# Kernel optimization log

Measured on AMD Instinct MI355X. Metric: run time of the kernel, lower is better.

## Reference

```python
import jax, jax.numpy as jnp
import numpy as np

N, E = 100000, 1000000
IN_DIM, OUT_DIM, HEADS = 64, 64, 4
C = OUT_DIM // HEADS  # per-head channels = 16
NEG_SLOPE = 0.2
SOFTMAX_EPS = 1e-16  # PyG softmax denominator epsilon
LN_EPS = 1e-5


def setup_inputs() -> dict:
    key = jax.random.key(0)
    ks = jax.random.split(key, 8)
    node_input = jax.random.normal(ks[0], (N, IN_DIM), dtype=jnp.float32)
    edge_index = jax.random.randint(ks[1], (2, E), 0, N, dtype=jnp.int64)
    # GATConv params (glorot-ish scale)
    W = jax.random.normal(ks[2], (IN_DIM, HEADS * C), dtype=jnp.float32) / np.sqrt(IN_DIM)
    att_src = jax.random.normal(ks[3], (HEADS, C), dtype=jnp.float32) / np.sqrt(C)
    att_dst = jax.random.normal(ks[4], (HEADS, C), dtype=jnp.float32) / np.sqrt(C)
    bias = jnp.zeros((HEADS * C,), dtype=jnp.float32)
    # LayerNorm params
    gamma = jnp.ones((OUT_DIM,), dtype=jnp.float32)
    beta = jnp.zeros((OUT_DIM,), dtype=jnp.float32)
    return {"node_input": node_input, "edge_index": edge_index, "W": W,
            "att_src": att_src, "att_dst": att_dst, "bias": bias,
            "gamma": gamma, "beta": beta}


def _gat_forward(x, edge_index, W, att_src, att_dst, bias, gamma, beta):
    src, dst = edge_index[0], edge_index[1]  # message flows src -> dst
    h = (x @ W).reshape(N, HEADS, C)                       # [N, H, C]
    a_src = jnp.einsum('nhc,hc->nh', h, att_src)           # [N, H]
    a_dst = jnp.einsum('nhc,hc->nh', h, att_dst)           # [N, H]
    # per-edge attention logits + leaky relu
    e = a_src[src] + a_dst[dst]                            # [E, H]
    e = jnp.where(e >= 0, e, NEG_SLOPE * e)
    # segment softmax over incoming edges of each target node
    m = jax.ops.segment_max(e, dst, num_segments=N)        # [N, H]
    m = jnp.where(jnp.isfinite(m), m, 0.0)                 # empty segments -> 0
    ex = jnp.exp(e - m[dst])                               # [E, H]
    denom = jax.ops.segment_sum(ex, dst, num_segments=N)   # [N, H]
    alpha = ex / (denom[dst] + SOFTMAX_EPS)                # [E, H]
    # weighted scatter-sum of source features
    msg = alpha[:, :, None] * h[src]                       # [E, H, C]
    out = jax.ops.segment_sum(msg, dst, num_segments=N)    # [N, H, C]
    out = out.reshape(N, HEADS * C) + bias                 # concat heads + bias
    # LayerNorm
    mu = out.mean(axis=-1, keepdims=True)
    var = out.var(axis=-1, keepdims=True)
    out = (out - mu) * jax.lax.rsqrt(var + LN_EPS) * gamma + beta
    # query gate is dead code (graph is a dict -> hasattr fails); dropout is eval identity
    return out


def reference(node_input, edge_index, W, att_src, att_dst, bias, gamma, beta):
    return _gat_forward(node_input, edge_index, W, att_src, att_dst, bias, gamma, beta)
```

## Files before the change

kernel.cpp:

```cpp
#include <hip/hip_runtime.h>
#include <hip/hip_bf16.h>
#include <math.h>

#define N_NODES 100000
#define E_EDGES 1000000
#define HEADS 4
#define DIM 64
#define NEG_SLOPE 0.2f
#define SM_EPS 1e-16f
#define LN_EPS 1e-5f
#define P1_BLOCKS 256
#define NT16 6250
#define GEMM_BLOCKS 1563
#define FEAT_BLOCKS (P1_BLOCKS + GEMM_BLOCKS)
#define CHUNK 3907
#define EPT 16
#define BUCKET_W 512
#define NBUCK 196
#define CAP 48

typedef __attribute__((ext_vector_type(8))) short short8v;
typedef __attribute__((ext_vector_type(4))) float f32x4;

static __device__ __forceinline__ unsigned short bfh(float f) {
    __hip_bfloat16 b = __float2bfloat16(f);
    return *reinterpret_cast<unsigned short*>(&b);
}
static __device__ __forceinline__ float bfh2f(unsigned short u) {
    return __uint_as_float((unsigned)u << 16);
}

__global__ __launch_bounds__(256) void k_wprep(
        const float* __restrict__ W, uint4* __restrict__ Wf) {
    int t = threadIdx.x;
    for (int e = t; e < 1024; e += 256) {
        int l = e & 63, f = e >> 6;
        int s = f & 1, kh = (f >> 1) & 1, n = f >> 2;
        int c = n * 16 + (l & 15);
        int k0 = kh * 32 + (l >> 4) * 8;
        unsigned short hw[8];
#pragma unroll
        for (int j = 0; j < 8; ++j) {
            float wv = W[(k0 + j) * 64 + c];
            unsigned short hi = bfh(wv);
            hw[j] = s ? bfh(wv - bfh2f(hi)) : hi;
        }
        uint4 pk;
        pk.x = hw[0] | ((unsigned)hw[1] << 16);
        pk.y = hw[2] | ((unsigned)hw[3] << 16);
        pk.z = hw[4] | ((unsigned)hw[5] << 16);
        pk.w = hw[6] | ((unsigned)hw[7] << 16);
        Wf[e] = pk;
    }
}

__global__ __launch_bounds__(256) void k_feat(
        const float* __restrict__ x, const float* __restrict__ Wf_,
        const float* __restrict__ att_src, const float* __restrict__ att_dst,
        const int* __restrict__ ei, __hip_bfloat16* __restrict__ hb,
        float* __restrict__ asrc, float* __restrict__ adst,
        int2* __restrict__ chunkbuf, int* __restrict__ pre) {
    __shared__ __align__(16) int smem_i[8326];
    int t = threadIdx.x;

    if (blockIdx.x < P1_BLOCKS) {
        int2* out2 = (int2*)smem_i;
        int*  cnt  = smem_i + 2 * CHUNK;
        int*  scan = cnt + 256;
        int base_e = blockIdx.x * CHUNK;
        int es[EPT], ed[EPT];
#pragma unroll
        for (int k = 0; k < EPT; ++k) {
            int i = k * 256 + t;
            int e = base_e + i;
            bool v = (i < CHUNK) && (e < E_EDGES);
            es[k] = v ? ei[e] : 0;
            ed[k] = v ? ei[E_EDGES + e] : -1;
        }
        cnt[t] = 0;
        __syncthreads();
#pragma unroll
        for (int k = 0; k < EPT; ++k)
            if (ed[k] >= 0) atomicAdd(&cnt[ed[k] >> 9], 1);
        __syncthreads();
        scan[t] = (t < NBUCK) ? cnt[t] : 0;
        __syncthreads();
#pragma unroll
        for (int off = 1; off < 256; off <<= 1) {
            int v = (t >= off) ? scan[t - off] : 0;
            __syncthreads();
            scan[t] += v;
            __syncthreads();
        }
        int excl = (t == 0) ? 0 : scan[t - 1];
        if (t < NBUCK) pre[blockIdx.x * (NBUCK + 1) + t] = excl;
        if (t == 0)    pre[blockIdx.x * (NBUCK + 1) + NBUCK] = scan[NBUCK - 1];
        if (t < NBUCK) cnt[t] = excl;
        __syncthreads();
#pragma unroll
        for (int k = 0; k < EPT; ++k)
            if (ed[k] >= 0) {
                int pos = atomicAdd(&cnt[ed[k] >> 9], 1);
                out2[pos] = make_int2(es[k], ed[k]);
            }
        __syncthreads();
        int ec = E_EDGES - base_e; ec = (ec > CHUNK) ? CHUNK : ec;
        for (int i = t; i < ec; i += 256)
            chunkbuf[base_e + i] = out2[i];
        return;
    }

    int w = t >> 6, lane = t & 63;
    int tile = (blockIdx.x - P1_BLOCKS) * 4 + w;
    if (tile >= NT16) return;
    int base = tile * 16;
    int m = lane & 15, kg = lane >> 4;

    const float* xr = x + (size_t)(base + m) * 64 + kg * 8;
    short8v ah[2], al[2];
#pragma unroll
    for (int kh = 0; kh < 2; ++kh) {
        float4 q0 = *(const float4*)(xr + kh * 32);
        float4 q1 = *(const float4*)(xr + kh * 32 + 4);
        float qq[8] = {q0.x, q0.y, q0.z, q0.w, q1.x, q1.y, q1.z, q1.w};
#pragma unroll
        for (int j = 0; j < 8; ++j) {
            unsigned short h = bfh(qq[j]);
            ah[kh][j] = (short)h;
            al[kh][j] = (short)bfh(qq[j] - bfh2f(h));
        }
    }

    const short8v* Wfv = (const short8v*)Wf_;
    float vs_keep = 0.f, vd_keep = 0.f;
#pragma unroll
    for (int n = 0; n < 4; ++n) {
        short8v bh0 = Wfv[((n * 2 + 0) * 2 + 0) * 64 + lane];
        short8v bl0 = Wfv[((n * 2 + 0) * 2 + 1) * 64 + lane];
        short8v bh1 = Wfv[((n * 2 + 1) * 2 + 0) * 64 + lane];
        short8v bl1 = Wfv[((n * 2 + 1) * 2 + 1) * 64 + lane];
        f32x4 a4 = {0.f, 0.f, 0.f, 0.f};
        a4 = __builtin_amdgcn_mfma_f32_16x16x32_bf16(ah[0], bh0, a4, 0, 0, 0);
        a4 = __builtin_amdgcn_mfma_f32_16x16x32_bf16(al[0], bh0, a4, 0, 0, 0);
        a4 = __builtin_amdgcn_mfma_f32_16x16x32_bf16(ah[0], bl0, a4, 0, 0, 0);
        a4 = __builtin_amdgcn_mfma_f32_16x16x32_bf16(ah[1], bh1, a4, 0, 0, 0);
        a4 = __builtin_amdgcn_mfma_f32_16x16x32_bf16(al[1], bh1, a4, 0, 0, 0);
        a4 = __builtin_amdgcn_mfma_f32_16x16x32_bf16(ah[1], bl1, a4, 0, 0, 0);
        float asv = att_src[n * 16 + m];
        float adv = att_dst[n * 16 + m];
#pragma unroll
        for (int ri = 0; ri < 4; ++ri) {
            int orow = base + kg * 4 + ri;
            hb[(size_t)orow * 64 + n * 16 + m] = __float2bfloat16(a4[ri]);
            float p = a4[ri] * asv, pd = a4[ri] * adv;
#pragma unroll
            for (int off = 1; off < 16; off <<= 1) {
                p  += __shfl_xor(p,  off, 64);
                pd += __shfl_xor(pd, off, 64);
            }
            if (m == ri * 4 + n) { vs_keep = p; vd_keep = pd; }
        }
    }
    asrc[tile * 64 + kg * 16 + m] = vs_keep;
    adst[tile * 64 + kg * 16 + m] = vd_keep;
}

__global__ __launch_bounds__(256) void k_bin2(
        const int2* __restrict__ chunkbuf, const int* __restrict__ pre,
        int* __restrict__ cursor, int* __restrict__ srclist) {
    __shared__ int cnt2[BUCKET_W];
    __shared__ int segstart[P1_BLOCKS];
    __shared__ int segpre[P1_BLOCKS + 1];
    __shared__ int scan[P1_BLOCKS];
    int t = threadIdx.x;
    int b = blockIdx.x;
    int base = b * BUCKET_W;
    for (int i = t; i < BUCKET_W; i += 256) cnt2[i] = 0;
    int p0 = pre[t * (NBUCK + 1) + b];
    int p1 = pre[t * (NBUCK + 1) + b + 1];
    segstart[t] = t * CHUNK + p0;
    scan[t] = p1 - p0;
    __syncthreads();
#pragma unroll
    for (int off = 1; off < 256; off <<= 1) {
        int v = (t >= off) ? scan[t - off] : 0;
        __syncthreads();
        scan[t] += v;
        __syncthreads();
    }
    segpre[t + 1] = scan[t];
    if (t == 0) segpre[0] = 0;
    __syncthreads();
    int total = segpre[P1_BLOCKS];
    for (int i = t; i < total; i += 256) {
        int lo = 0, hi = P1_BLOCKS;
#pragma unroll
        for (int it = 0; it < 8; ++it) {
            int mid = (lo + hi) >> 1;
            if (segpre[mid] <= i) lo = mid; else hi = mid;
        }
        int2 e = chunkbuf[segstart[lo] + (i - segpre[lo])];
        int pos = atomicAdd(&cnt2[e.y - base], 1);
        if (pos < CAP) srclist[e.y * CAP + pos] = e.x;
    }
    __syncthreads();
    for (int i = t; i < BUCKET_W; i += 256) {
        int node = base + i;
        if (node < N_NODES) cursor[node] = cnt2[i];
    }
}

__global__ __launch_bounds__(256) void k_aggr(
        const int* __restrict__ cursor, const int* __restrict__ srclist,
        const float* __restrict__ asrc, const float* __restrict__ adst,
        const __hip_bfloat16* __restrict__ hb,
        const float* __restrict__ bias, const float* __restrict__ gamma,
        const float* __restrict__ beta, float* __restrict__ out) {
    int t = threadIdx.x;
    int node = blockIdx.x * 4 + (t >> 6);
    int lane = t & 63;
    int q = lane >> 4, j = lane & 15;
    int hd = j >> 2;
    int dcnt = cursor[node];
    dcnt = (dcnt > CAP) ? CAP : dcnt;
    const int* sl = srclist + node * CAP;
    const ushort4* hp = (const ushort4*)hb;
    float ad = adst[node * HEADS + hd];
    float acc0 = 0.f, acc1 = 0.f, acc2 = 0.f, acc3 = 0.f, l = 0.f;

    for (int i0 = 0; i0 < dcnt; i0 += 16) {
        int idx[4];
        float as[4];
        ushort4 hv[4];
#pragma unroll
        for (int k = 0; k < 4; ++k) {
            int ek = i0 + 4 * k + q;
            idx[k] = (ek < dcnt) ? sl[ek] : 0;
        }
#pragma unroll
        for (int k = 0; k < 4; ++k) as[k] = asrc[idx[k] * HEADS + hd];
#pragma unroll
        for (int k = 0; k < 4; ++k) hv[k] = hp[idx[k] * 16 + j];
#pragma unroll
        for (int k = 0; k < 4; ++k) {
            int ek = i0 + 4 * k + q;
            float e = as[k] + ad;
            e = (e >= 0.f) ? e : NEG_SLOPE * e;
            float p = (ek < dcnt) ? __expf(e) : 0.f;
            l += p;
            acc0 += p * __uint_as_float((unsigned)hv[k].x << 16);
            acc1 += p * __uint_as_float((unsigned)hv[k].y << 16);
            acc2 += p * __uint_as_float((unsigned)hv[k].z << 16);
            acc3 += p * __uint_as_float((unsigned)hv[k].w << 16);
        }
    }
    acc0 += __shfl_xor(acc0, 16, 64); acc0 += __shfl_xor(acc0, 32, 64);
    acc1 += __shfl_xor(acc1, 16, 64); acc1 += __shfl_xor(acc1, 32, 64);
    acc2 += __shfl_xor(acc2, 16, 64); acc2 += __shfl_xor(acc2, 32, 64);
    acc3 += __shfl_xor(acc3, 16, 64); acc3 += __shfl_xor(acc3, 32, 64);
    l    += __shfl_xor(l,    16, 64); l    += __shfl_xor(l,    32, 64);

    float inv = 1.f / (l + SM_EPS);
    float4 b4 = ((const float4*)bias)[j];
    float v0 = acc0 * inv + b4.x;
    float v1 = acc1 * inv + b4.y;
    float v2 = acc2 * inv + b4.z;
    float v3 = acc3 * inv + b4.w;
    float s1 = (v0 + v1) + (v2 + v3);
    float s2 = (v0 * v0 + v1 * v1) + (v2 * v2 + v3 * v3);
#pragma unroll
    for (int off = 1; off < 16; off <<= 1) {
        s1 += __shfl_xor(s1, off, 64);
        s2 += __shfl_xor(s2, off, 64);
    }
    float mu = s1 * (1.f / 64.f);
    float var = s2 * (1.f / 64.f) - mu * mu;
    float r = rsqrtf(var + LN_EPS);
    if (q == 0) {
        float4 g4 = ((const float4*)gamma)[j];
        float4 be4 = ((const float4*)beta)[j];
        float4 o;
        o.x = (v0 - mu) * r * g4.x + be4.x;
        o.y = (v1 - mu) * r * g4.y + be4.y;
        o.z = (v2 - mu) * r * g4.z + be4.z;
        o.w = (v3 - mu) * r * g4.w + be4.w;
        ((float4*)(out + (size_t)node * DIM))[j] = o;
    }
}

extern "C" void kernel_launch(void* const* d_in, const int* in_sizes, int n_in,
                              void* d_out, int out_size, void* d_ws, size_t ws_size,
                              hipStream_t stream) {
    const float* x       = (const float*)d_in[0];
    const int*   ei      = (const int*)d_in[1];
    const float* W       = (const float*)d_in[2];
    const float* att_src = (const float*)d_in[3];
    const float* att_dst = (const float*)d_in[4];
    const float* bias    = (const float*)d_in[5];
    const float* gamma   = (const float*)d_in[6];
    const float* beta    = (const float*)d_in[7];
    float* out = (float*)d_out;

    int2* chunkbuf = (int2*)d_ws;
    int*  pre      = (int*)(chunkbuf + (size_t)P1_BLOCKS * CHUNK);
    int*  cursor   = pre + (size_t)P1_BLOCKS * (NBUCK + 1);
    int*  srclist  = cursor + N_NODES;
    float* asrc    = (float*)(srclist + (size_t)N_NODES * CAP);
    float* adst    = asrc + (size_t)N_NODES * HEADS;
    __hip_bfloat16* hb = (__hip_bfloat16*)(adst + (size_t)N_NODES * HEADS);
    uint4* Wf      = (uint4*)(hb + (size_t)N_NODES * DIM);

    k_wprep<<<1, 256, 0, stream>>>(W, Wf);
    k_feat<<<FEAT_BLOCKS, 256, 0, stream>>>(x, (const float*)Wf, att_src,
                                            att_dst, ei, hb, asrc, adst,
                                            chunkbuf, pre);
    k_bin2<<<NBUCK, 256, 0, stream>>>(chunkbuf, pre, cursor, srclist);
    k_aggr<<<N_NODES / 4, 256, 0, stream>>>(cursor, srclist, asrc, adst, hb,
                                            bias, gamma, beta, out);
}
```

Baseline: 167.2 us.

## Build compact CSR source lists and pack two nodes per wavefront in aggregation

The binning kernel now runs two passes over each bucket's edges. The first pass counts in-degree per node, then an in-block prefix scan plus a global bucket offset gives exact CSR offsets, packed with the degree into one cursor word. This replaces the fixed 48-slot padded per-node list, which shrinks the source-list footprint and removes the silent cap. The aggregation kernel now gives each wavefront two nodes of 32 lanes each, iterating to the larger of the two degrees, so low-degree nodes waste fewer lanes. In exchange, binning reads the chunk buffer twice, and the packed word limits the degree to 63.

```diff
diff --git a/kernel.cpp b/kernel.cpp
--- a/kernel.cpp
+++ b/kernel.cpp
@@ -17,7 +17,6 @@
 #define EPT 16
 #define BUCKET_W 512
 #define NBUCK 196
-#define CAP 48
 
 typedef __attribute__((ext_vector_type(8))) short short8v;
 typedef __attribute__((ext_vector_type(4))) float f32x4;
@@ -167,18 +166,29 @@
 
 __global__ __launch_bounds__(256) void k_bin2(
         const int2* __restrict__ chunkbuf, const int* __restrict__ pre,
-        int* __restrict__ cursor, int* __restrict__ srclist) {
+        int* __restrict__ cursorP, int* __restrict__ srclist) {
     __shared__ int cnt2[BUCKET_W];
     __shared__ int segstart[P1_BLOCKS];
     __shared__ int segpre[P1_BLOCKS + 1];
     __shared__ int scan[P1_BLOCKS];
     int t = threadIdx.x;
     int b = blockIdx.x;
-    int base = b * BUCKET_W;
+    int nbase = b * BUCKET_W;
     for (int i = t; i < BUCKET_W; i += 256) cnt2[i] = 0;
     int p0 = pre[t * (NBUCK + 1) + b];
     int p1 = pre[t * (NBUCK + 1) + b + 1];
     segstart[t] = t * CHUNK + p0;
+    scan[t] = p0;
+    __syncthreads();
+#pragma unroll
+    for (int off = 128; off >= 1; off >>= 1) {
+        int v = (t < off) ? scan[t + off] : 0;
+        __syncthreads();
+        if (t < off) scan[t] += v;
+        __syncthreads();
+    }
+    int gbase = scan[0];
+    __syncthreads();
     scan[t] = p1 - p0;
     __syncthreads();
 #pragma unroll
@@ -200,41 +210,65 @@
             if (segpre[mid] <= i) lo = mid; else hi = mid;
         }
         int2 e = chunkbuf[segstart[lo] + (i - segpre[lo])];
-        int pos = atomicAdd(&cnt2[e.y - base], 1);
-        if (pos < CAP) srclist[e.y * CAP + pos] = e.x;
-    }
-    __syncthreads();
-    for (int i = t; i < BUCKET_W; i += 256) {
-        int node = base + i;
-        if (node < N_NODES) cursor[node] = cnt2[i];
+        atomicAdd(&cnt2[e.y - nbase], 1);
+    }
+    __syncthreads();
+    int c0 = cnt2[2 * t], c1 = cnt2[2 * t + 1];
+    scan[t] = c0 + c1;
+    __syncthreads();
+#pragma unroll
+    for (int off = 1; off < 256; off <<= 1) {
+        int v = (t >= off) ? scan[t - off] : 0;
+        __syncthreads();
+        scan[t] += v;
+        __syncthreads();
+    }
+    int pexcl = (t == 0) ? 0 : scan[t - 1];
+    cnt2[2 * t]     = pexcl;
+    cnt2[2 * t + 1] = pexcl + c0;
+    int n0 = nbase + 2 * t;
+    if (n0 < N_NODES)     cursorP[n0]     = ((gbase + pexcl) << 6) | c0;
+    if (n0 + 1 < N_NODES) cursorP[n0 + 1] = ((gbase + pexcl + c0) << 6) | c1;
+    __syncthreads();
+    for (int i = t; i < total; i += 256) {
+        int lo = 0, hi = P1_BLOCKS;
+#pragma unroll
+        for (int it = 0; it < 8; ++it) {
+            int mid = (lo + hi) >> 1;
+            if (segpre[mid] <= i) lo = mid; else hi = mid;
+        }
+        int2 e = chunkbuf[segstart[lo] + (i - segpre[lo])];
+        int pos = atomicAdd(&cnt2[e.y - nbase], 1);
+        srclist[gbase + pos] = e.x;
     }
 }
 
 __global__ __launch_bounds__(256) void k_aggr(
-        const int* __restrict__ cursor, const int* __restrict__ srclist,
+        const int* __restrict__ cursorP, const int* __restrict__ srclist,
         const float* __restrict__ asrc, const float* __restrict__ adst,
         const __hip_bfloat16* __restrict__ hb,
         const float* __restrict__ bias, const float* __restrict__ gamma,
         const float* __restrict__ beta, float* __restrict__ out) {
     int t = threadIdx.x;
-    int node = blockIdx.x * 4 + (t >> 6);
     int lane = t & 63;
-    int q = lane >> 4, j = lane & 15;
+    int s = lane >> 5, qq = (lane >> 4) & 1, j = lane & 15;
     int hd = j >> 2;
-    int dcnt = cursor[node];
-    dcnt = (dcnt > CAP) ? CAP : dcnt;
-    const int* sl = srclist + node * CAP;
+    int node = blockIdx.x * 8 + (t >> 6) * 2 + s;
+    int cw = cursorP[node];
+    int dcnt = cw & 63;
+    const int* sl = srclist + ((unsigned)cw >> 6);
+    int dmax = max(dcnt, __shfl_xor(dcnt, 32, 64));
     const ushort4* hp = (const ushort4*)hb;
     float ad = adst[node * HEADS + hd];
     float acc0 = 0.f, acc1 = 0.f, acc2 = 0.f, acc3 = 0.f, l = 0.f;
 
-    for (int i0 = 0; i0 < dcnt; i0 += 16) {
+    for (int i0 = 0; i0 < dmax; i0 += 8) {
         int idx[4];
         float as[4];
         ushort4 hv[4];
 #pragma unroll
         for (int k = 0; k < 4; ++k) {
-            int ek = i0 + 4 * k + q;
+            int ek = i0 + 2 * k + qq;
             idx[k] = (ek < dcnt) ? sl[ek] : 0;
         }
 #pragma unroll
@@ -243,7 +277,7 @@
         for (int k = 0; k < 4; ++k) hv[k] = hp[idx[k] * 16 + j];
 #pragma unroll
         for (int k = 0; k < 4; ++k) {
-            int ek = i0 + 4 * k + q;
+            int ek = i0 + 2 * k + qq;
             float e = as[k] + ad;
             e = (e >= 0.f) ? e : NEG_SLOPE * e;
             float p = (ek < dcnt) ? __expf(e) : 0.f;
@@ -254,11 +288,11 @@
             acc3 += p * __uint_as_float((unsigned)hv[k].w << 16);
         }
     }
-    acc0 += __shfl_xor(acc0, 16, 64); acc0 += __shfl_xor(acc0, 32, 64);
-    acc1 += __shfl_xor(acc1, 16, 64); acc1 += __shfl_xor(acc1, 32, 64);
-    acc2 += __shfl_xor(acc2, 16, 64); acc2 += __shfl_xor(acc2, 32, 64);
-    acc3 += __shfl_xor(acc3, 16, 64); acc3 += __shfl_xor(acc3, 32, 64);
-    l    += __shfl_xor(l,    16, 64); l    += __shfl_xor(l,    32, 64);
+    acc0 += __shfl_xor(acc0, 16, 64);
+    acc1 += __shfl_xor(acc1, 16, 64);
+    acc2 += __shfl_xor(acc2, 16, 64);
+    acc3 += __shfl_xor(acc3, 16, 64);
+    l    += __shfl_xor(l,    16, 64);
 
     float inv = 1.f / (l + SM_EPS);
     float4 b4 = ((const float4*)bias)[j];
@@ -276,7 +310,7 @@
     float mu = s1 * (1.f / 64.f);
     float var = s2 * (1.f / 64.f) - mu * mu;
     float r = rsqrtf(var + LN_EPS);
-    if (q == 0) {
+    if (qq == 0) {
         float4 g4 = ((const float4*)gamma)[j];
         float4 be4 = ((const float4*)beta)[j];
         float4 o;
@@ -303,9 +337,9 @@
 
     int2* chunkbuf = (int2*)d_ws;
     int*  pre      = (int*)(chunkbuf + (size_t)P1_BLOCKS * CHUNK);
-    int*  cursor   = pre + (size_t)P1_BLOCKS * (NBUCK + 1);
-    int*  srclist  = cursor + N_NODES;
-    float* asrc    = (float*)(srclist + (size_t)N_NODES * CAP);
+    int*  cursorP  = pre + (size_t)P1_BLOCKS * (NBUCK + 1);
+    int*  srclist  = cursorP + N_NODES;
+    float* asrc    = (float*)(srclist + (size_t)E_EDGES);
     float* adst    = asrc + (size_t)N_NODES * HEADS;
     __hip_bfloat16* hb = (__hip_bfloat16*)(adst + (size_t)N_NODES * HEADS);
     uint4* Wf      = (uint4*)(hb + (size_t)N_NODES * DIM);
@@ -314,7 +348,7 @@
     k_feat<<<FEAT_BLOCKS, 256, 0, stream>>>(x, (const float*)Wf, att_src,
                                             att_dst, ei, hb, asrc, adst,
                                             chunkbuf, pre);
-    k_bin2<<<NBUCK, 256, 0, stream>>>(chunkbuf, pre, cursor, srclist);
-    k_aggr<<<N_NODES / 4, 256, 0, stream>>>(cursor, srclist, asrc, adst, hb,
+    k_bin2<<<NBUCK, 256, 0, stream>>>(chunkbuf, pre, cursorP, srclist);
+    k_aggr<<<N_NODES / 8, 256, 0, stream>>>(cursorP, srclist, asrc, adst, hb,
                                             bias, gamma, beta, out);
 }
```

New measurement: 166.9 us. No clear change (-0.2%).
